# Optimization experiments

Measured on AMD Instinct MI355X. Metric: run time of the kernel, lower is better.

## Reference

```python
import jax, jax.numpy as jnp
import numpy as np

N, E0 = 50000, 800000          # nodes, raw edges (self-loops appended in reference)
IN, H, C = 128, 8, 8           # in_channels, heads, out_channels per head
ED, T = 16, 96                 # edge_dim, temporal profile length
NEG_SLOPE = 0.2                # leaky relu slope
CW = 0.5                       # complementarity_weight


def setup_inputs() -> dict:
    key = jax.random.key(0)
    ks = jax.random.split(key, 12)
    def xavier(k, shape):
        fan_in, fan_out = shape[1], shape[0]
        lim = np.sqrt(6.0 / (fan_in + fan_out)).astype(np.float32)
        return jax.random.uniform(k, shape, jnp.float32, -lim, lim)
    return {
        "x": jax.random.normal(ks[0], (N, IN), jnp.float32),
        "edge_index": jax.random.randint(ks[1], (2, E0), 0, N, jnp.int64),
        "edge_attr": jax.random.normal(ks[2], (E0, ED), jnp.float32),
        "temporal_profiles": jax.random.normal(ks[3], (N, T), jnp.float32),
        "Wq": xavier(ks[4], (H * C, IN)),
        "Wk": xavier(ks[5], (H * C, IN)),
        "Wv": xavier(ks[6], (H * C, IN)),
        "We": xavier(ks[7], (H * C, ED)),
        "comp_W": xavier(ks[8], (H, 2 * IN)),
        "comp_b": jnp.zeros((H,), jnp.float32),
        "Wo": xavier(ks[9], (C, H * C)),
        "bo": jnp.zeros((C,), jnp.float32),
    }


def reference(x, edge_index, edge_attr, temporal_profiles,
              Wq, Wk, Wv, We, comp_W, comp_b, Wo, bo):
    n = x.shape[0]
    # ---- add self loops (PyG add_self_loops; edge_attr filled with 1.0) ----
    loops = jnp.arange(n, dtype=edge_index.dtype)
    ei = jnp.concatenate([edge_index, jnp.stack([loops, loops])], axis=1)
    ea = jnp.concatenate(
        [edge_attr, jnp.ones((n, edge_attr.shape[1]), edge_attr.dtype)], axis=0)
    src, dst = ei[0], ei[1]  # key/value side (j) = src, query side (i) = dst

    # ---- node projections [N, H, C] ----
    q = (x @ Wq.T).reshape(n, H, C)
    k = (x @ Wk.T).reshape(n, H, C)
    v = (x @ Wv.T).reshape(n, H, C)

    # ---- complementarity scores per edge ----
    tp = temporal_profiles
    tpn = (tp - tp.mean(axis=1, keepdims=True)) / \
          (tp.std(axis=1, ddof=1, keepdims=True) + 1e-8)  # torch std is unbiased
    correlation = (tpn[src] * tpn[dst]).mean(axis=1)       # [E]
    # Linear(2*IN -> H) on concat([x[src], x[dst]]) == split matmul per node
    a_node = x @ comp_W[:, :IN].T                          # [N, H]
    b_node = x @ comp_W[:, IN:].T                          # [N, H]
    learned = jnp.tanh(a_node[src] + b_node[dst] + comp_b).mean(axis=1)
    comp = 0.5 * correlation + 0.5 * learned               # [E]

    # ---- per-edge attention logits ----
    key_j = k[src]                                         # [E, H, C]
    alpha = (q[dst] * key_j).sum(-1) / np.sqrt(C).astype(np.float32)  # [E, H]
    edge_feat = (ea @ We.T).reshape(-1, H, C)
    alpha = alpha + (edge_feat * key_j).sum(-1)
    alpha = alpha + CW * (-comp)[:, None]
    alpha = jnp.where(alpha >= 0, alpha, NEG_SLOPE * alpha)  # leaky_relu

    # ---- segment softmax over destination nodes (PyG softmax) ----
    amax = jax.ops.segment_max(alpha, dst, num_segments=n)   # every node has a self loop
    e = jnp.exp(alpha - amax[dst])
    denom = jax.ops.segment_sum(e, dst, num_segments=n)
    att = e / (denom[dst] + 1e-16)                           # [E, H]

    # ---- weighted scatter-add aggregation ----
    msg = v[src] * att[:, :, None]                           # [E, H, C]
    out = jax.ops.segment_sum(msg, dst, num_segments=n).reshape(n, H * C)
    return out @ Wo.T + bo
```

## Files before the change

kernel.cpp:

```cpp
#include <hip/hip_runtime.h>
#include <math.h>


struct __align__(8) US4 { unsigned short x, y, z, w; };

typedef __attribute__((ext_vector_type(8))) short bf16x8;
typedef __attribute__((ext_vector_type(4))) float f32x4;

#define CH 32

__device__ __forceinline__ unsigned short f2bf(float f) {
    unsigned u = __float_as_uint(f);
    unsigned r = (u + 0x7fffu + ((u >> 16) & 1u)) >> 16;
    return (unsigned short)r;
}
__device__ __forceinline__ float bf2f(unsigned short u) {
    return __uint_as_float(((unsigned)u) << 16);
}
__device__ __forceinline__ float blo(unsigned u) { return __uint_as_float(u << 16); }
__device__ __forceinline__ float bhi(unsigned u) { return __uint_as_float(u & 0xffff0000u); }

__global__ __launch_bounds__(256) void k_bpack(
    const float* __restrict__ Wq, const float* __restrict__ Wk, const float* __restrict__ Wv,
    const float* __restrict__ compW, const float* __restrict__ We,
    unsigned short* __restrict__ Bp)
{
    int gid = blockIdx.x * 256 + threadIdx.x;
    if (gid >= 21 * 2048) return;
    int i = gid & 7, lane = (gid >> 3) & 63, s = (gid >> 9) & 3, t = gid >> 11;
    int col = t * 16 + (lane & 15);
    int k = s * 32 + ((lane >> 4) << 3) + i;
    float v;
    if (col < 64)        v = Wq[col * 128 + k];
    else if (col < 128)  v = Wk[(col - 64) * 128 + k];
    else if (col < 192)  v = Wv[(col - 128) * 128 + k];
    else if (col < 200)  v = compW[(col - 192) * 256 + k];
    else if (col < 208)  v = compW[(col - 200) * 256 + 128 + k];
    else {
        int hd = col - 208, h = hd >> 4, d = hd & 15;
        v = 0.f;
        #pragma unroll
        for (int c = 0; c < 8; c++)
            v += Wk[(h * 8 + c) * 128 + k] * We[(h * 8 + c) * 16 + d];
    }
    Bp[gid] = f2bf(v);
}

__device__ __forceinline__ bf16x8 ld_bf8(const float* p) {
    float4 a = ((const float4*)p)[0], b = ((const float4*)p)[1];
    bf16x8 r;
    r[0] = (short)f2bf(a.x); r[1] = (short)f2bf(a.y);
    r[2] = (short)f2bf(a.z); r[3] = (short)f2bf(a.w);
    r[4] = (short)f2bf(b.x); r[5] = (short)f2bf(b.y);
    r[6] = (short)f2bf(b.z); r[7] = (short)f2bf(b.w);
    return r;
}

__global__ __launch_bounds__(256) void k_gemm(
    const float* __restrict__ x, const unsigned short* __restrict__ Bp,
    const float* __restrict__ compb,
    float* __restrict__ q, unsigned short* __restrict__ rec,
    float* __restrict__ bnArr, int N)
{
    const int tid = threadIdx.x, w = tid >> 6, lane = tid & 63;
    const int half = lane >> 4;
    const int c0 = lane & 15;
    int row_a = blockIdx.x * 64 + w * 16 + c0;
    int ra = min(row_a, N - 1);
    const float* xr = x + (size_t)ra * 128 + half * 8;
    bf16x8 a0 = ld_bf8(xr +  0);
    bf16x8 a1 = ld_bf8(xr + 32);
    bf16x8 a2 = ld_bf8(xr + 64);
    bf16x8 a3 = ld_bf8(xr + 96);
    const int rbase = blockIdx.x * 64 + w * 16 + half * 4;
    const float cbv = compb[c0 & 7];

    for (int t = 0; t < 21; t++) {
        f32x4 acc = {0.f, 0.f, 0.f, 0.f};
        const bf16x8* bp = (const bf16x8*)(Bp + (size_t)((t * 4) * 64 + lane) * 8);
        acc = __builtin_amdgcn_mfma_f32_16x16x32_bf16(a0, bp[0],   acc, 0, 0, 0);
        acc = __builtin_amdgcn_mfma_f32_16x16x32_bf16(a1, bp[64],  acc, 0, 0, 0);
        acc = __builtin_amdgcn_mfma_f32_16x16x32_bf16(a2, bp[128], acc, 0, 0, 0);
        acc = __builtin_amdgcn_mfma_f32_16x16x32_bf16(a3, bp[192], acc, 0, 0, 0);
        #pragma unroll
        for (int r = 0; r < 4; r++) {
            int rr = rbase + r;
            if (rr >= N) continue;
            float vr = acc[r];
            unsigned short* recR = rec + (size_t)rr * 320;
            if (t < 4)        q[(size_t)rr * 64 + t * 16 + c0] = vr * 0.35355339059327373f;
            else if (t < 8)   recR[(t - 4) * 16 + c0] = f2bf(vr);
            else if (t < 12)  recR[192 + (t - 8) * 16 + c0] = f2bf(vr);
            else if (t == 12) {
                if (c0 < 8) ((float*)(recR + 304))[c0] = vr;
                else        bnArr[(size_t)rr * 8 + (c0 - 8)] = vr + cbv;
            }
            else              recR[64 + (t - 13) * 16 + c0] = f2bf(vr);
        }
    }
}

__global__ __launch_bounds__(256) void k_tpn(const float* __restrict__ tp,
                                             unsigned short* __restrict__ rec, int N)
{
    int wave = threadIdx.x >> 6;
    int lane = threadIdx.x & 63;
    int n = blockIdx.x * 4 + wave;
    if (n >= N) return;
    const float* row = tp + (size_t)n * 96;
    float v0 = row[lane];
    float v1 = (lane < 32) ? row[64 + lane] : 0.f;
    float s = v0 + v1, ss = v0 * v0 + v1 * v1;
    #pragma unroll
    for (int m = 1; m < 64; m <<= 1) { s += __shfl_xor(s, m); ss += __shfl_xor(ss, m); }
    float mean = s * (1.f / 96.f);
    float var = (ss - 96.f * mean * mean) * (1.f / 95.f);
    var = fmaxf(var, 0.f);
    float inv = 12.f / (sqrtf(var) + 1e-8f);
    if (lane < 24) {
        float4 v = ((const float4*)row)[lane];
        int q0 = (int)rintf(fminf(fmaxf((v.x - mean) * inv, -127.f), 127.f));
        int q1 = (int)rintf(fminf(fmaxf((v.y - mean) * inv, -127.f), 127.f));
        int q2 = (int)rintf(fminf(fmaxf((v.z - mean) * inv, -127.f), 127.f));
        int q3 = (int)rintf(fminf(fmaxf((v.w - mean) * inv, -127.f), 127.f));
        unsigned pk = (q0 & 255) | ((q1 & 255) << 8) | ((q2 & 255) << 16) | ((q3 & 255) << 24);
        *((unsigned*)(rec + (size_t)n * 320 + 256) + lane) = pk;
    }
}

__global__ __launch_bounds__(256) void k_hist(const int* __restrict__ ei,
                                              int* __restrict__ deg,
                                              int* __restrict__ rnk, int E0, int N)
{
    int e = blockIdx.x * 256 + threadIdx.x;
    int E = E0 + N;
    if (e >= E) return;
    int dst = (e < E0) ? ei[E0 + e] : (e - E0);
    rnk[e] = atomicAdd(&deg[dst], 1);
}

__global__ __launch_bounds__(256) void k_scanA(const int* __restrict__ deg,
                                               int* __restrict__ bsum, int N)
{
    __shared__ int sm[256];
    int i = blockIdx.x * 256 + threadIdx.x;
    sm[threadIdx.x] = (i < N) ? deg[i] : 0;
    __syncthreads();
    for (int off = 128; off > 0; off >>= 1) {
        if (threadIdx.x < off) sm[threadIdx.x] += sm[threadIdx.x + off];
        __syncthreads();
    }
    if (threadIdx.x == 0) bsum[blockIdx.x] = sm[0];
}

__global__ __launch_bounds__(256) void k_scanB(int* __restrict__ bsum, int NB)
{
    __shared__ int sm[256];
    int t = threadIdx.x;
    sm[t] = (t < NB) ? bsum[t] : 0;
    __syncthreads();
    for (int off = 1; off < 256; off <<= 1) {
        int v = (t >= off) ? sm[t - off] : 0;
        __syncthreads();
        sm[t] += v;
        __syncthreads();
    }
    if (t < NB) bsum[t] = (t == 0) ? 0 : sm[t - 1];
}

__global__ __launch_bounds__(256) void k_scanC(const int* __restrict__ deg,
                                               const int* __restrict__ bsum,
                                               int* __restrict__ row, int N)
{
    __shared__ int sm[256];
    int b = blockIdx.x, t = threadIdx.x, i = b * 256 + t;
    int v = (i < N) ? deg[i] : 0;
    sm[t] = v;
    __syncthreads();
    for (int off = 1; off < 256; off <<= 1) {
        int u = (t >= off) ? sm[t - off] : 0;
        __syncthreads();
        sm[t] += u;
        __syncthreads();
    }
    int excl = bsum[b] + sm[t] - v;
    if (i < N) {
        row[i] = excl;
        if (i == N - 1) row[N] = excl + v;
    }
}

__global__ __launch_bounds__(256) void k_scatter(const int* __restrict__ ei,
                                                 const int* __restrict__ row,
                                                 const int* __restrict__ rnk,
                                                 int2* __restrict__ csrd, int E0, int N)
{
    int e = blockIdx.x * 256 + threadIdx.x;
    int E = E0 + N;
    if (e >= E) return;
    int src, dst;
    if (e < E0) { src = ei[e]; dst = ei[E0 + e]; }
    else        { src = e - E0; dst = src; }
    int pos = row[dst] + rnk[e];
    csrd[pos] = make_int2(e, src);
}

__global__ __launch_bounds__(256) void k_nodeattn(
    const int2* __restrict__ csrd, const int* __restrict__ row,
    const float* __restrict__ eattr,
    const float* __restrict__ q, const unsigned short* __restrict__ rec,
    const float* __restrict__ bnArr,
    const float* __restrict__ Wo, const float* __restrict__ bo,
    float* __restrict__ out, int E0, int N)
{
    const int tid = threadIdx.x;
    const int wave = tid >> 6, lane = tid & 63;
    const int n = blockIdx.x * 4 + wave;
    if (n >= N) return;

    const int beg = row[n], end = row[n + 1];
    const int h = lane & 7;
    const int g = lane >> 3;
    const int koff = h * 8;
    const int goff = 64 + h * 16;
    const int voff = 192 + h * 8;

    const unsigned short* recN = rec + (size_t)n * 320;
    const float4* qp = (const float4*)(q + (size_t)n * 64 + h * 8);
    const float4 qd0 = qp[0], qd1 = qp[1];
    const float bnh = bnArr[(size_t)n * 8 + h];
    const unsigned* tdq = (const unsigned*)(recN + 256) + h * 3;
    const int y0 = (int)tdq[0], y1 = (int)tdq[1], y2 = (int)tdq[2];
    const float CC = -0.25f / (96.f * 144.f);

    float m_reg = -1e30f, dsum = 0.f;
    float acc[8];
    #pragma unroll
    for (int c = 0; c < 8; c++) acc[c] = 0.f;

    for (int cbeg = beg; cbeg < end; cbeg += CH) {
        const int cnt = min(CH, end - cbeg);

        float av[4];
        uint4 vu[4];
        #pragma unroll
        for (int j = 0; j < 4; j++) {
            av[j] = -1e30f;
            vu[j] = make_uint4(0u, 0u, 0u, 0u);
            int eo = g + 8 * j;
            if (eo < cnt) {
                int2 es = csrd[cbeg + eo];
                const int e = es.x, s = es.y;
                const unsigned short* recS = rec + (size_t)s * 320;

                vu[j] = *(const uint4*)(recS + voff);

                const US4* kp = (const US4*)(recS + koff);
                US4 k0 = kp[0], k1 = kp[1];
                float qk = qd0.x*bf2f(k0.x) + qd0.y*bf2f(k0.y) + qd0.z*bf2f(k0.z) + qd0.w*bf2f(k0.w)
                         + qd1.x*bf2f(k1.x) + qd1.y*bf2f(k1.y) + qd1.z*bf2f(k1.z) + qd1.w*bf2f(k1.w);

                const uint4* gp = (const uint4*)(recS + goff);
                uint4 g0 = gp[0], g1 = gp[1];
                int ec = (e < E0) ? e : 0;
                const float4* ep4 = (const float4*)(eattr + (size_t)ec * 16);
                float4 e0 = ep4[0], e1 = ep4[1], e2 = ep4[2], e3 = ep4[3];
                if (e >= E0) {
                    e0 = make_float4(1.f, 1.f, 1.f, 1.f); e1 = e0; e2 = e0; e3 = e0;
                }
                float efk = e0.x*blo(g0.x) + e0.y*bhi(g0.x) + e0.z*blo(g0.y) + e0.w*bhi(g0.y)
                          + e1.x*blo(g0.z) + e1.y*bhi(g0.z) + e1.z*blo(g0.w) + e1.w*bhi(g0.w)
                          + e2.x*blo(g1.x) + e2.y*bhi(g1.x) + e2.z*blo(g1.y) + e2.w*bhi(g1.y)
                          + e3.x*blo(g1.z) + e3.y*bhi(g1.z) + e3.z*blo(g1.w) + e3.w*bhi(g1.w);

                float tv = ((const float*)(recS + 304))[h] + bnh;
                float ex = __expf(2.f * tv);
                float tn = 1.f - 2.f / (ex + 1.f);

                const unsigned* tsq = (const unsigned*)(recS + 256) + h * 3;
                unsigned x0 = tsq[0], x1 = tsq[1], x2 = tsq[2];
#if __has_builtin(__builtin_amdgcn_sdot4)
                int di = __builtin_amdgcn_sdot4((int)x0, y0, 0, false);
                di = __builtin_amdgcn_sdot4((int)x1, y1, di, false);
                di = __builtin_amdgcn_sdot4((int)x2, y2, di, false);
                float pc = (float)di * CC;
#else
                float pc =
                    (float)((int)(x0 << 24) >> 24) * (float)((int)(y0 << 24) >> 24)
                  + (float)((int)(x0 << 16) >> 24) * (float)((int)(y0 << 16) >> 24)
                  + (float)((int)(x0 <<  8) >> 24) * (float)((int)(y0 <<  8) >> 24)
                  + (float)((int)x0 >> 24)         * (float)((int)y0 >> 24)
                  + (float)((int)(x1 << 24) >> 24) * (float)((int)(y1 << 24) >> 24)
                  + (float)((int)(x1 << 16) >> 24) * (float)((int)(y1 << 16) >> 24)
                  + (float)((int)(x1 <<  8) >> 24) * (float)((int)(y1 <<  8) >> 24)
                  + (float)((int)x1 >> 24)         * (float)((int)y1 >> 24)
                  + (float)((int)(x2 << 24) >> 24) * (float)((int)(y2 << 24) >> 24)
                  + (float)((int)(x2 << 16) >> 24) * (float)((int)(y2 << 16) >> 24)
                  + (float)((int)(x2 <<  8) >> 24) * (float)((int)(y2 <<  8) >> 24)
                  + (float)((int)x2 >> 24)         * (float)((int)y2 >> 24);
                pc *= CC;
#endif
                float cv = pc + tn * (-0.25f / 8.f);
                cv += __shfl_xor(cv, 1); cv += __shfl_xor(cv, 2); cv += __shfl_xor(cv, 4);

                float a = qk + efk + cv;
                av[j] = fmaxf(a, 0.2f * a);
            }
        }

        float mloc = fmaxf(fmaxf(av[0], av[1]), fmaxf(av[2], av[3]));
        mloc = fmaxf(mloc, __shfl_xor(mloc, 8));
        mloc = fmaxf(mloc, __shfl_xor(mloc, 16));
        mloc = fmaxf(mloc, __shfl_xor(mloc, 32));

        float mn = fmaxf(m_reg, mloc);
        float sc = __expf(m_reg - mn);
        m_reg = mn;
        dsum *= sc;
        #pragma unroll
        for (int c = 0; c < 8; c++) acc[c] *= sc;

        #pragma unroll
        for (int j = 0; j < 4; j++) {
            float p = __expf(av[j] - mn);
            dsum += p;
            acc[0] += p * blo(vu[j].x); acc[1] += p * bhi(vu[j].x);
            acc[2] += p * blo(vu[j].y); acc[3] += p * bhi(vu[j].y);
            acc[4] += p * blo(vu[j].z); acc[5] += p * bhi(vu[j].z);
            acc[6] += p * blo(vu[j].w); acc[7] += p * bhi(vu[j].w);
        }
    }

    dsum += __shfl_xor(dsum, 8); dsum += __shfl_xor(dsum, 16); dsum += __shfl_xor(dsum, 32);
    #pragma unroll
    for (int c = 0; c < 8; c++) {
        acc[c] += __shfl_xor(acc[c], 8);
        acc[c] += __shfl_xor(acc[c], 16);
        acc[c] += __shfl_xor(acc[c], 32);
    }
    float inv = 1.f / (dsum + 1e-16f);

    float po[8];
    #pragma unroll
    for (int cp8 = 0; cp8 < 8; cp8++) {
        const float4* wr = (const float4*)(Wo + cp8 * 64 + h * 8);
        float4 w0 = wr[0], w1 = wr[1];
        po[cp8] = inv * (acc[0]*w0.x + acc[1]*w0.y + acc[2]*w0.z + acc[3]*w0.w
                       + acc[4]*w1.x + acc[5]*w1.y + acc[6]*w1.z + acc[7]*w1.w);
    }
    #pragma unroll
    for (int cp8 = 0; cp8 < 8; cp8++) {
        po[cp8] += __shfl_xor(po[cp8], 1);
        po[cp8] += __shfl_xor(po[cp8], 2);
        po[cp8] += __shfl_xor(po[cp8], 4);
    }
    if (lane < 8) out[(size_t)n * 8 + lane] = po[lane] + bo[lane];
}

extern "C" void kernel_launch(void* const* d_in, const int* in_sizes, int n_in,
                              void* d_out, int out_size, void* d_ws, size_t ws_size,
                              hipStream_t stream)
{
    const float* x     = (const float*)d_in[0];
    const int*   ei    = (const int*)d_in[1];
    const float* eattr = (const float*)d_in[2];
    const float* tp    = (const float*)d_in[3];
    const float* Wq    = (const float*)d_in[4];
    const float* Wk    = (const float*)d_in[5];
    const float* Wv    = (const float*)d_in[6];
    const float* We    = (const float*)d_in[7];
    const float* compW = (const float*)d_in[8];
    const float* compb = (const float*)d_in[9];
    const float* Wo    = (const float*)d_in[10];
    const float* bo    = (const float*)d_in[11];
    float* out = (float*)d_out;

    const int N  = in_sizes[0] / 128;
    const int E0 = in_sizes[1] / 2;
    const int E  = E0 + N;
    const int NB = (N + 255) / 256;

    float* ws = (float*)d_ws;
    size_t off = 0;
    unsigned short* rec = (unsigned short*)(ws + off); off += (size_t)N * 160;
    float* q  = ws + off; off += (size_t)N * 64;
    float* bnArr = ws + off; off += (size_t)N * 8;
    int* deg    = (int*)(ws + off); off += N;
    int* bsum   = (int*)(ws + off); off += 256;
    int* rowp   = (int*)(ws + off); off += N + 4;
    unsigned short* Bp = (unsigned short*)(ws + off); off += 21504;
    int2* csrd  = (int2*)(ws + off); off += (size_t)E * 2;
    int* rnk    = (int*)(ws + off); off += E;

    hipMemsetAsync(deg, 0, (size_t)N * sizeof(int), stream);

    k_hist<<<(E + 255) / 256, 256, 0, stream>>>(ei, deg, rnk, E0, N);
    k_scanA<<<NB, 256, 0, stream>>>(deg, bsum, N);
    k_scanB<<<1, 256, 0, stream>>>(bsum, NB);
    k_scanC<<<NB, 256, 0, stream>>>(deg, bsum, rowp, N);
    k_scatter<<<(E + 255) / 256, 256, 0, stream>>>(ei, rowp, rnk, csrd, E0, N);

    k_bpack<<<(21 * 2048 + 255) / 256, 256, 0, stream>>>(Wq, Wk, Wv, compW, We, Bp);
    k_gemm<<<(N + 63) / 64, 256, 0, stream>>>(x, Bp, compb, q, rec, bnArr, N);
    k_tpn<<<(N + 3) / 4, 256, 0, stream>>>(tp, rec, N);

    k_nodeattn<<<(N + 3) / 4, 256, 0, stream>>>(csrd, rowp, eattr, q, rec, bnArr,
                                                Wo, bo, out, E0, N);
}
```

Baseline: 201.0 us.

## Process nodes in descending-degree order via counting-sort permutation

Adds a counting sort of nodes by in-degree (histogram, scan, scatter) and has the attention kernel process nodes through this permutation, heaviest first. The goal is to balance the four waves in each block and reduce tail imbalance from skewed degrees. The cost is three extra small launches, atomics, and an extra indirection that makes node-indexed accesses less coalesced. With uniform random edges the degree spread is narrow, so the balancing gain may be small.

```diff
diff --git a/kernel.cpp b/kernel.cpp
--- a/kernel.cpp
+++ b/kernel.cpp
@@ -205,7 +205,44 @@
     csrd[pos] = make_int2(e, src);
 }
 
+__global__ __launch_bounds__(256) void k_dhist(const int* __restrict__ deg,
+                                               int* __restrict__ dh, int N)
+{
+    int n = blockIdx.x * 256 + threadIdx.x;
+    if (n >= N) return;
+    atomicAdd(&dh[255 - min(deg[n], 255)], 1);
+}
+
+__global__ __launch_bounds__(256) void k_dscan(int* __restrict__ dh, int* __restrict__ dbase)
+{
+    __shared__ int sm[256];
+    int t = threadIdx.x;
+    sm[t] = dh[t];
+    __syncthreads();
+    for (int off = 1; off < 256; off <<= 1) {
+        int v = (t >= off) ? sm[t - off] : 0;
+        __syncthreads();
+        sm[t] += v;
+        __syncthreads();
+    }
+    dbase[t] = (t == 0) ? 0 : sm[t - 1];
+    dh[t] = 0;
+}
+
+__global__ __launch_bounds__(256) void k_dscatter(const int* __restrict__ deg,
+                                                  const int* __restrict__ dbase,
+                                                  int* __restrict__ dcur,
+                                                  int* __restrict__ perm, int N)
+{
+    int n = blockIdx.x * 256 + threadIdx.x;
+    if (n >= N) return;
+    int b = 255 - min(deg[n], 255);
+    int p = dbase[b] + atomicAdd(&dcur[b], 1);
+    perm[p] = n;
+}
+
 __global__ __launch_bounds__(256) void k_nodeattn(
+    const int* __restrict__ perm,
     const int2* __restrict__ csrd, const int* __restrict__ row,
     const float* __restrict__ eattr,
     const float* __restrict__ q, const unsigned short* __restrict__ rec,
@@ -215,8 +252,9 @@
 {
     const int tid = threadIdx.x;
     const int wave = tid >> 6, lane = tid & 63;
-    const int n = blockIdx.x * 4 + wave;
-    if (n >= N) return;
+    const int nIdx = blockIdx.x * 4 + wave;
+    if (nIdx >= N) return;
+    const int n = perm[nIdx];
 
     const int beg = row[n], end = row[n + 1];
     const int h = lane & 7;
@@ -386,13 +424,16 @@
     float* q  = ws + off; off += (size_t)N * 64;
     float* bnArr = ws + off; off += (size_t)N * 8;
     int* deg    = (int*)(ws + off); off += N;
+    int* dh     = (int*)(ws + off); off += 256;
+    int* dbase  = (int*)(ws + off); off += 256;
+    int* perm   = (int*)(ws + off); off += N;
     int* bsum   = (int*)(ws + off); off += 256;
     int* rowp   = (int*)(ws + off); off += N + 4;
     unsigned short* Bp = (unsigned short*)(ws + off); off += 21504;
     int2* csrd  = (int2*)(ws + off); off += (size_t)E * 2;
     int* rnk    = (int*)(ws + off); off += E;
 
-    hipMemsetAsync(deg, 0, (size_t)N * sizeof(int), stream);
+    hipMemsetAsync(deg, 0, (size_t)(N + 256) * sizeof(int), stream);
 
     k_hist<<<(E + 255) / 256, 256, 0, stream>>>(ei, deg, rnk, E0, N);
     k_scanA<<<NB, 256, 0, stream>>>(deg, bsum, N);
@@ -400,10 +441,14 @@
     k_scanC<<<NB, 256, 0, stream>>>(deg, bsum, rowp, N);
     k_scatter<<<(E + 255) / 256, 256, 0, stream>>>(ei, rowp, rnk, csrd, E0, N);
 
+    k_dhist<<<NB, 256, 0, stream>>>(deg, dh, N);
+    k_dscan<<<1, 256, 0, stream>>>(dh, dbase);
+    k_dscatter<<<NB, 256, 0, stream>>>(deg, dbase, dh, perm, N);
+
     k_bpack<<<(21 * 2048 + 255) / 256, 256, 0, stream>>>(Wq, Wk, Wv, compW, We, Bp);
     k_gemm<<<(N + 63) / 64, 256, 0, stream>>>(x, Bp, compb, q, rec, bnArr, N);
     k_tpn<<<(N + 3) / 4, 256, 0, stream>>>(tp, rec, N);
 
-    k_nodeattn<<<(N + 3) / 4, 256, 0, stream>>>(csrd, rowp, eattr, q, rec, bnArr,
+    k_nodeattn<<<(N + 3) / 4, 256, 0, stream>>>(perm, csrd, rowp, eattr, q, rec, bnArr,
                                                 Wo, bo, out, E0, N);
 }
```

Measured after the change: 449.2 us. 123% more time.
